# Kernel optimization log

Hardware: AMD Instinct MI355X
Metric: run time of the kernel (lower is better)

Reference implementation:

```python
import jax, jax.numpy as jnp
import numpy as np

NHEADS = 16
KVHEADS = 4
HEAD_DIM = 128  # emb_kq_per_head == emb_v_per_head
ROPE_THETA = 10000.0


def _rotary(x, cos, sin):
    # x: [B, S, H, D]; half-split rotation
    x1, x2 = jnp.split(x, 2, axis=-1)
    rot = jnp.concatenate([-x2, x1], axis=-1)
    return x * cos + rot * sin


def setup_inputs() -> dict:
    key = jax.random.key(0)
    k1, k2, k3 = jax.random.split(key, 3)
    B, S, E = 2, 2048, 2048
    qkv_out = NHEADS * HEAD_DIM + 2 * KVHEADS * HEAD_DIM  # 3072
    return {
        "x": jax.random.normal(k1, (B, S, E), dtype=jnp.float32),
        "w_qkv": jax.random.normal(k2, (E, qkv_out), dtype=jnp.float32) * 0.02,
        "w_dense": jax.random.normal(k3, (NHEADS * HEAD_DIM, E), dtype=jnp.float32) * 0.02,
    }


def reference(x, w_qkv, w_dense):
    B, S, E = x.shape
    D = HEAD_DIM
    # fused QKV projection (use_bias=False), then split per FusedQKV.splits
    qkv = x @ w_qkv  # [B, S, 3072]
    q, k, v = jnp.split(qkv, [NHEADS * D, NHEADS * D + KVHEADS * D], axis=-1)
    q = q.reshape(B, S, NHEADS, D)
    k = k.reshape(B, S, KVHEADS, D)
    v = v.reshape(B, S, KVHEADS, D)

    # rotary position encoding, positions = arange(S)
    pos = jnp.arange(S, dtype=jnp.float32)
    inv_freq = 1.0 / (ROPE_THETA ** (jnp.arange(0, D, 2, dtype=jnp.float32) / D))
    ang = pos[:, None] * inv_freq[None, :]                 # [S, D/2]
    ang = jnp.concatenate([ang, ang], axis=-1)             # [S, D]
    cos = jnp.cos(ang)[None, :, None, :]                   # [1, S, 1, D]
    sin = jnp.sin(ang)[None, :, None, :]
    q = _rotary(q, cos, sin)
    k = _rotary(k, cos, sin)

    # GQA: expand kv heads to query heads
    rep = NHEADS // KVHEADS
    k = jnp.repeat(k, rep, axis=2)  # [B, S, NHEADS, D]
    v = jnp.repeat(v, rep, axis=2)

    scale = 1.0 / jnp.sqrt(jnp.asarray(D, dtype=x.dtype))
    scores = jnp.einsum("bqhd,bkhd->bhqk", q, k) * scale   # [B, H, S, S]
    causal = jnp.tril(jnp.ones((S, S), dtype=bool))
    scores = jnp.where(causal[None, None], scores, jnp.finfo(scores.dtype).min)
    probs = jax.nn.softmax(scores, axis=-1)
    attn = jnp.einsum("bhqk,bkhd->bqhd", probs, v)         # [B, S, H, D]
    attn = attn.reshape(B, S, NHEADS * D)
    return attn @ w_dense                                  # [B, S, E]
```

## Files before the change

kernel.cpp:

```cpp
#include <hip/hip_runtime.h>
#include <type_traits>


typedef __attribute__((ext_vector_type(8))) short short8;
typedef __attribute__((ext_vector_type(4))) float floatx4;
typedef __attribute__((ext_vector_type(4))) unsigned short ushort4v;

constexpr int NH    = 16;
constexpr int NKV   = 4;
constexpr int HD    = 128;
constexpr int SEQ   = 2048;
constexpr int EMB   = 2048;
constexpr int NBATCH = 2;
constexpr int MROWS = NBATCH * SEQ;
constexpr int NQKV  = (NH + 2 * NKV) * HD;

__device__ __forceinline__ unsigned short f2b(float f) {
  union { float f; unsigned u; } v; v.f = f;
  unsigned u = v.u + 0x7FFFu + ((v.u >> 16) & 1u);
  return (unsigned short)(u >> 16);
}
__device__ __forceinline__ float b2f(unsigned short h) {
  union { unsigned u; float f; } v; v.u = (unsigned)h << 16;
  return v.f;
}

__device__ __forceinline__ void gload_lds16(const unsigned short* g,
                                            unsigned short* lds) {
  __builtin_amdgcn_global_load_lds(
      (const __attribute__((address_space(1))) unsigned int*)g,
      (__attribute__((address_space(3))) unsigned int*)lds, 16, 0, 0);
}

__global__ void cvt_f32_bf16(const float* __restrict__ in,
                             unsigned short* __restrict__ out, int n) {
  int i = (blockIdx.x * 256 + threadIdx.x) * 4;
  if (i + 3 < n) {
    floatx4 v = *(const floatx4*)(in + i);
    ushort4v o = { f2b(v[0]), f2b(v[1]), f2b(v[2]), f2b(v[3]) };
    *(ushort4v*)(out + i) = o;
  }
}

__global__ void transpose_cvt_f32(const float* __restrict__ in,
                                  unsigned short* __restrict__ out,
                                  int R, int C) {
  __shared__ float t[32][33];
  int c0 = blockIdx.x * 32, r0 = blockIdx.y * 32;
  int tx = threadIdx.x & 31, ty = threadIdx.x >> 5;
#pragma unroll
  for (int i = 0; i < 32; i += 8)
    t[ty + i][tx] = in[(long)(r0 + ty + i) * C + (c0 + tx)];
  __syncthreads();
#pragma unroll
  for (int i = 0; i < 32; i += 8)
    out[(long)(c0 + ty + i) * R + (r0 + tx)] = f2b(t[tx][ty + i]);
}

__global__ void transpose_bf16(const unsigned short* __restrict__ in,
                               unsigned short* __restrict__ out,
                               int R, int C) {
  __shared__ unsigned short t[32][34];
  long base = (long)blockIdx.z * R * C;
  in += base; out += base;
  int c0 = blockIdx.x * 32, r0 = blockIdx.y * 32;
  int tx = threadIdx.x & 31, ty = threadIdx.x >> 5;
#pragma unroll
  for (int i = 0; i < 32; i += 8)
    t[ty + i][tx] = in[(long)(r0 + ty + i) * C + (c0 + tx)];
  __syncthreads();
#pragma unroll
  for (int i = 0; i < 32; i += 8)
    out[(long)(c0 + ty + i) * R + (r0 + tx)] = t[tx][ty + i];
}

__global__ void rope_kernel(unsigned short* __restrict__ buf, float scale) {
  int idx = blockIdx.x * 256 + threadIdx.x;
  int i = idx & 63;
  int s = (idx >> 6) & (SEQ - 1);
  int bh = idx >> 17;
  unsigned short* p = buf + ((long)bh * SEQ + s) * HD;
  float e = -(float)i * (2.0f * 13.287712379549449f / 128.0f);
  float ang = (float)s * exp2f(e);
  float sn, c;
  sincosf(ang, &sn, &c);
  float x1 = b2f(p[i]), x2 = b2f(p[i + 64]);
  p[i]      = f2b((x1 * c - x2 * sn) * scale);
  p[i + 64] = f2b((x2 * c + x1 * sn) * scale);
}

constexpr int BM = 128, BN = 128, BK = 64;

template <int MODE>
__global__ __launch_bounds__(256, 2) void gemm_bt(
    const unsigned short* __restrict__ A,
    const unsigned short* __restrict__ BT,
    int Mdim, int Ndim, int Kdim,
    float* __restrict__ outF,
    unsigned short* __restrict__ Qb,
    unsigned short* __restrict__ Kb,
    unsigned short* __restrict__ Vb) {
  __shared__ __align__(16) unsigned short smem[BM * BK + BN * BK];
  unsigned short (*As)[BK] = (unsigned short (*)[BK])smem;
  unsigned short (*Bs)[BK] = (unsigned short (*)[BK])(smem + BM * BK);
  const int tid = threadIdx.x;
  const int bm = blockIdx.y * BM;
  const int bn = blockIdx.x * BN;
  const int wave = tid >> 6, lane = tid & 63;
  const int l = lane & 15, q = lane >> 4;
  const int wm = (wave >> 1) * 64, wn = (wave & 1) * 64;

  floatx4 acc[4][4] = {};

  const int srow = lane >> 3;
  const int scol = (lane & 7) * 8;
  const unsigned short* Arow = A + (long)bm * Kdim;
  const unsigned short* Brow = BT + (long)bn * Kdim;

  for (int k0 = 0; k0 < Kdim; k0 += BK) {
#pragma unroll
    for (int i = 0; i < 4; ++i) {
      const int r0 = wave * 32 + i * 8;
      gload_lds16(Arow + (long)(r0 + srow) * Kdim + k0 + scol, &As[r0][0]);
      gload_lds16(Brow + (long)(r0 + srow) * Kdim + k0 + scol, &Bs[r0][0]);
    }
    __syncthreads();
#pragma unroll
    for (int kk = 0; kk < 2; ++kk) {
      short8 af[4], bfr[4];
#pragma unroll
      for (int mi = 0; mi < 4; ++mi)
        af[mi] = *(const short8*)&As[wm + mi * 16 + l][kk * 32 + q * 8];
#pragma unroll
      for (int ni = 0; ni < 4; ++ni)
        bfr[ni] = *(const short8*)&Bs[wn + ni * 16 + l][kk * 32 + q * 8];
#pragma unroll
      for (int mi = 0; mi < 4; ++mi)
#pragma unroll
        for (int ni = 0; ni < 4; ++ni)
          acc[mi][ni] = __builtin_amdgcn_mfma_f32_16x16x32_bf16(
              af[mi], bfr[ni], acc[mi][ni], 0, 0, 0);
    }
    __syncthreads();
  }

  if constexpr (MODE == 1) {
#pragma unroll
    for (int mi = 0; mi < 4; ++mi) {
      const int rowbase = bm + wm + mi * 16 + q * 4;
#pragma unroll
      for (int ni = 0; ni < 4; ++ni) {
        const int col = bn + wn + ni * 16 + l;
#pragma unroll
        for (int r = 0; r < 4; ++r)
          outF[(long)(rowbase + r) * Ndim + col] = acc[mi][ni][r];
      }
    }
  } else {
    unsigned short (*Ct)[128] = (unsigned short (*)[128])smem;
#pragma unroll
    for (int mi = 0; mi < 4; ++mi)
#pragma unroll
      for (int ni = 0; ni < 4; ++ni)
#pragma unroll
        for (int r = 0; r < 4; ++r) {
          const int row = wm + mi * 16 + q * 4 + r;
          const int col = wn + ni * 16 + l;
          const int cs = ((((col >> 3) ^ row) & 7) | (col & 64 ? 8 : 0)) * 8 + (col & 7);
          Ct[row][cs] = f2b(acc[mi][ni][r]);
        }
    __syncthreads();
    const int row = tid >> 1, g = tid & 1;
    const int m = bm + row, bb = m >> 11, s = m & (SEQ - 1);
    unsigned short* dst;
    if (bn < NH * HD)
      dst = Qb + (((long)(bb * NH + (bn >> 7))) * SEQ + s) * HD;
    else if (bn < (NH + NKV) * HD)
      dst = Kb + (((long)(bb * NKV + ((bn - NH * HD) >> 7))) * SEQ + s) * HD;
    else
      dst = Vb + (((long)(bb * NKV + ((bn - (NH + NKV) * HD) >> 7))) * SEQ + s) * HD;
#pragma unroll
    for (int i = 0; i < 8; ++i) {
      const int blk = (g * 8) + (i ^ (row & 7));
      *(short8*)(dst + g * 64 + i * 8) = *(const short8*)&Ct[row][blk * 8];
    }
  }
}

__global__ __launch_bounds__(256, 2) void attn_kernel(
    const unsigned short* __restrict__ Q,
    const unsigned short* __restrict__ K,
    const unsigned short* __restrict__ VT,
    unsigned short* __restrict__ attn) {
  const int pair = blockIdx.x, h = blockIdx.y, b = blockIdx.z;
  const int kvh = h >> 2;
  const int tid = threadIdx.x;
  const int wave = tid >> 6, lane = tid & 63;
  const int l = lane & 15, q = lane >> 4;
  const int l7 = l & 7;
  const int wq = wave * 16;

  const unsigned short* Kh = K + ((long)(b * NKV + kvh)) * SEQ * HD;
  const unsigned short* VTh = VT + ((long)(b * NKV + kvh)) * HD * SEQ;

  __shared__ __align__(16) unsigned short Ks[2][64 * 128];
  __shared__ __align__(16) unsigned short VTs[2][144 * 64];
  __shared__ __align__(16) unsigned short Ps[64][72];

  int koff[4], voff[4];
  {
    const int k_rl = lane >> 4, k_bp = lane & 15;
    const int v_rl = lane >> 3, v_bp = lane & 7;
#pragma unroll
    for (int j = 0; j < 4; ++j) {
      const int rk = (wave * 4 + j) * 4 + k_rl;
      koff[j] = rk * HD + (k_bp ^ (rk & 15)) * 8;
      const int rv = (wave * 4 + j) * 8 + v_rl;
      voff[j] = rv * SEQ + (v_bp ^ (rv & 7)) * 8;
    }
  }

  {
    short8 onesv;
#pragma unroll
    for (int i = 0; i < 8; ++i) onesv[i] = (short)0x3F80;
    const int t8 = tid * 8;
    unsigned short* dstp = (t8 < 1024) ? &VTs[0][128 * 64 + t8]
                                       : &VTs[1][128 * 64 + (t8 - 1024)];
    *(short8*)dstp = onesv;
  }

  auto stage = [&](int c, int buf) {
    const unsigned short* kc = Kh + c * (64 * HD);
    const unsigned short* vc = VTh + c * 64;
#pragma unroll
    for (int j = 0; j < 4; ++j)
      gload_lds16(kc + koff[j], &Ks[buf][(wave * 4 + j) * 4 * 128]);
#pragma unroll
    for (int j = 0; j < 4; ++j)
      gload_lds16(vc + voff[j], &VTs[buf][(wave * 4 + j) * 8 * 64]);
  };

  auto chunk_body = [&](auto masked, int cur, int kv0, int qt,
                        short8* qf, floatx4* o, float* mrow) {
    constexpr bool MASKED = decltype(masked)::value;
    floatx4 sf[4] = {};
#pragma unroll
    for (int kk = 0; kk < 4; ++kk) {
      short8 kf[4];
#pragma unroll
      for (int ni = 0; ni < 4; ++ni) {
        const int row = ni * 16 + l;
        kf[ni] = *(const short8*)&Ks[cur][row * 128 + (((kk * 4 + q) ^ l) * 8)];
      }
#pragma unroll
      for (int ni = 0; ni < 4; ++ni)
        sf[ni] = __builtin_amdgcn_mfma_f32_16x16x32_bf16(
            qf[kk], kf[ni], sf[ni], 0, 0, 0);
    }
    float alpha[4], mloc[4];
#pragma unroll
    for (int r = 0; r < 4; ++r) {
      if constexpr (MASKED) {
        const int qrow = qt * 64 + wq + q * 4 + r;
#pragma unroll
        for (int ni = 0; ni < 4; ++ni)
          if (kv0 + ni * 16 + l > qrow) sf[ni][r] = -3e38f;
      }
      float smax = fmaxf(fmaxf(sf[0][r], sf[1][r]), fmaxf(sf[2][r], sf[3][r]));
#pragma unroll
      for (int d = 1; d < 16; d <<= 1) smax = fmaxf(smax, __shfl_xor(smax, d));
      const float mnew = fmaxf(mrow[r], smax);
      alpha[r] = exp2f(mrow[r] - mnew);
      mrow[r] = mnew;
      mloc[r] = mnew;
    }
    floatx4 av = { alpha[0], alpha[1], alpha[2], alpha[3] };
#pragma unroll
    for (int di = 0; di < 9; ++di) o[di] *= av;
#pragma unroll
    for (int r = 0; r < 4; ++r)
#pragma unroll
      for (int ni = 0; ni < 4; ++ni)
        Ps[wq + q * 4 + r][ni * 16 + l] = f2b(exp2f(sf[ni][r] - mloc[r]));
#pragma unroll
    for (int kvk = 0; kvk < 2; ++kvk) {
      short8 pf = *(const short8*)&Ps[wq + l][kvk * 32 + q * 8];
#pragma unroll
      for (int di = 0; di < 9; ++di) {
        const int row = di * 16 + l;
        short8 vf = *(const short8*)&VTs[cur][row * 64 + (((kvk * 4 + q) ^ l7) * 8)];
        o[di] = __builtin_amdgcn_mfma_f32_16x16x32_bf16(pf, vf, o[di], 0, 0, 0);
      }
    }
  };

#pragma unroll 1
  for (int half = 0; half < 2; ++half) {
    const int qt = half ? (31 - pair) : pair;
    const unsigned short* Qh = Q + (((long)(b * NH + h)) * SEQ + qt * 64) * HD;

    short8 qf[4];
#pragma unroll
    for (int kk = 0; kk < 4; ++kk)
      qf[kk] = *(const short8*)(Qh + (long)(wq + l) * HD + kk * 32 + q * 8);

    floatx4 o[9] = {};
    float mrow[4];
#pragma unroll
    for (int r = 0; r < 4; ++r) mrow[r] = -3e38f;

    const int nchunk = qt + 1;

    stage(0, 0);
    __syncthreads();

    int c = 0;
#pragma unroll 1
    for (; c < nchunk - 1; ++c) {
      stage(c + 1, (c & 1) ^ 1);
      chunk_body(std::false_type{}, c & 1, c * 64, qt, qf, o, mrow);
      __syncthreads();
    }
    chunk_body(std::true_type{}, c & 1, c * 64, qt, qf, o, mrow);
    __syncthreads();

#pragma unroll
    for (int r = 0; r < 4; ++r) {
      const float inv = 1.0f / o[8][r];
      const int s = qt * 64 + wq + q * 4 + r;
      unsigned short* dst = attn + ((long)(b * SEQ + s)) * (NH * HD) + h * HD;
#pragma unroll
      for (int di = 0; di < 8; ++di)
        dst[di * 16 + l] = f2b(o[di][r] * inv);
    }
  }
}

extern "C" void kernel_launch(void* const* d_in, const int* in_sizes, int n_in,
                              void* d_out, int out_size, void* d_ws, size_t ws_size,
                              hipStream_t stream) {
  const float* x       = (const float*)d_in[0];
  const float* w_qkv   = (const float*)d_in[1];
  const float* w_dense = (const float*)d_in[2];
  float* out = (float*)d_out;

  char* ws = (char*)d_ws;
  const size_t MB = 1024 * 1024;
  unsigned short* xb    = (unsigned short*)(ws);
  unsigned short* wqkvT = (unsigned short*)(ws + 16 * MB);
  unsigned short* wdT   = (unsigned short*)(ws + 28 * MB);
  unsigned short* Qb    = (unsigned short*)(ws + 36 * MB);
  unsigned short* Kb    = (unsigned short*)(ws + 52 * MB);
  unsigned short* Vb    = (unsigned short*)(ws + 56 * MB);
  unsigned short* VTb   = (unsigned short*)(ws + 60 * MB);
  unsigned short* attn  = xb;

  const float qscale = 0.08838834764831845f * 1.4426950408889634f;

  cvt_f32_bf16<<<(MROWS * EMB) / (256 * 4), 256, 0, stream>>>(x, xb, MROWS * EMB);
  transpose_cvt_f32<<<dim3(NQKV / 32, EMB / 32), 256, 0, stream>>>(w_qkv, wqkvT, EMB, NQKV);
  transpose_cvt_f32<<<dim3(EMB / 32, (NH * HD) / 32), 256, 0, stream>>>(w_dense, wdT, NH * HD, EMB);

  gemm_bt<0><<<dim3(NQKV / BN, MROWS / BM), 256, 0, stream>>>(
      xb, wqkvT, MROWS, NQKV, EMB, nullptr, Qb, Kb, Vb);

  rope_kernel<<<(NBATCH * NH * SEQ * 64) / 256, 256, 0, stream>>>(Qb, qscale);
  rope_kernel<<<(NBATCH * NKV * SEQ * 64) / 256, 256, 0, stream>>>(Kb, 1.0f);

  transpose_bf16<<<dim3(HD / 32, SEQ / 32, NBATCH * NKV), 256, 0, stream>>>(Vb, VTb, SEQ, HD);

  attn_kernel<<<dim3(16, NH, NBATCH), 256, 0, stream>>>(Qb, Kb, VTb, attn);

  gemm_bt<1><<<dim3(EMB / BN, MROWS / BM), 256, 0, stream>>>(
      attn, wdT, MROWS, EMB, NH * HD, out, nullptr, nullptr, nullptr);
}
```

Measured before the change: 329.3 us.

## Read V directly from global in attention, one q-tile per block, merge rope launches

The attention kernel stops staging the transposed V tile in shared memory and instead loads V fragments straight from global memory into registers for the PV MFMAs. The row-sum column becomes an MFMA against a register vector of ones. Each block now handles a single query tile, heaviest first, instead of a balanced pair, doubling the grid and raising launch bounds to 3 blocks per CU thanks to the smaller LDS footprint. The two rope launches are merged into one. The risk is uncoalesced, higher-latency global V reads repeated by every wave, which is also 4x redundant across GQA heads.

```diff
diff --git a/kernel.cpp b/kernel.cpp
--- a/kernel.cpp
+++ b/kernel.cpp
@@ -74,12 +74,16 @@
     out[(long)(c0 + ty + i) * R + (r0 + tx)] = t[tx][ty + i];
 }
 
-__global__ void rope_kernel(unsigned short* __restrict__ buf, float scale) {
+__global__ void rope_kernel(unsigned short* __restrict__ Qb,
+                            unsigned short* __restrict__ Kb, float qscale) {
   int idx = blockIdx.x * 256 + threadIdx.x;
   int i = idx & 63;
   int s = (idx >> 6) & (SEQ - 1);
   int bh = idx >> 17;
-  unsigned short* p = buf + ((long)bh * SEQ + s) * HD;
+  unsigned short* p;
+  float scale;
+  if (bh < NBATCH * NH) { p = Qb + ((long)bh * SEQ + s) * HD; scale = qscale; }
+  else { p = Kb + ((long)(bh - NBATCH * NH) * SEQ + s) * HD; scale = 1.0f; }
   float e = -(float)i * (2.0f * 13.287712379549449f / 128.0f);
   float ang = (float)s * exp2f(e);
   float sn, c;
@@ -187,61 +191,48 @@
   }
 }
 
-__global__ __launch_bounds__(256, 2) void attn_kernel(
+__global__ __launch_bounds__(256, 3) void attn_kernel(
     const unsigned short* __restrict__ Q,
     const unsigned short* __restrict__ K,
     const unsigned short* __restrict__ VT,
     unsigned short* __restrict__ attn) {
-  const int pair = blockIdx.x, h = blockIdx.y, b = blockIdx.z;
+  const int qt = 31 - blockIdx.x, h = blockIdx.y, b = blockIdx.z;
   const int kvh = h >> 2;
   const int tid = threadIdx.x;
   const int wave = tid >> 6, lane = tid & 63;
   const int l = lane & 15, q = lane >> 4;
-  const int l7 = l & 7;
   const int wq = wave * 16;
 
   const unsigned short* Kh = K + ((long)(b * NKV + kvh)) * SEQ * HD;
   const unsigned short* VTh = VT + ((long)(b * NKV + kvh)) * HD * SEQ;
 
   __shared__ __align__(16) unsigned short Ks[2][64 * 128];
-  __shared__ __align__(16) unsigned short VTs[2][144 * 64];
   __shared__ __align__(16) unsigned short Ps[64][72];
 
-  int koff[4], voff[4];
+  int koff[4];
   {
     const int k_rl = lane >> 4, k_bp = lane & 15;
-    const int v_rl = lane >> 3, v_bp = lane & 7;
 #pragma unroll
     for (int j = 0; j < 4; ++j) {
       const int rk = (wave * 4 + j) * 4 + k_rl;
       koff[j] = rk * HD + (k_bp ^ (rk & 15)) * 8;
-      const int rv = (wave * 4 + j) * 8 + v_rl;
-      voff[j] = rv * SEQ + (v_bp ^ (rv & 7)) * 8;
-    }
-  }
-
-  {
-    short8 onesv;
-#pragma unroll
-    for (int i = 0; i < 8; ++i) onesv[i] = (short)0x3F80;
-    const int t8 = tid * 8;
-    unsigned short* dstp = (t8 < 1024) ? &VTs[0][128 * 64 + t8]
-                                       : &VTs[1][128 * 64 + (t8 - 1024)];
-    *(short8*)dstp = onesv;
-  }
+    }
+  }
+
+  short8 onesf;
+#pragma unroll
+  for (int i = 0; i < 8; ++i) onesf[i] = (short)0x3F80;
 
   auto stage = [&](int c, int buf) {
     const unsigned short* kc = Kh + c * (64 * HD);
-    const unsigned short* vc = VTh + c * 64;
 #pragma unroll
     for (int j = 0; j < 4; ++j)
       gload_lds16(kc + koff[j], &Ks[buf][(wave * 4 + j) * 4 * 128]);
-#pragma unroll
-    for (int j = 0; j < 4; ++j)
-      gload_lds16(vc + voff[j], &VTs[buf][(wave * 4 + j) * 8 * 64]);
   };
 
-  auto chunk_body = [&](auto masked, int cur, int kv0, int qt,
+  const unsigned short* vbase = VTh + (long)l * SEQ + q * 8;
+
+  auto chunk_body = [&](auto masked, int cur, int kv0,
                         short8* qf, floatx4* o, float* mrow) {
     constexpr bool MASKED = decltype(masked)::value;
     floatx4 sf[4] = {};
@@ -283,57 +274,52 @@
 #pragma unroll
       for (int ni = 0; ni < 4; ++ni)
         Ps[wq + q * 4 + r][ni * 16 + l] = f2b(exp2f(sf[ni][r] - mloc[r]));
+    const unsigned short* vc = vbase + kv0;
 #pragma unroll
     for (int kvk = 0; kvk < 2; ++kvk) {
       short8 pf = *(const short8*)&Ps[wq + l][kvk * 32 + q * 8];
 #pragma unroll
-      for (int di = 0; di < 9; ++di) {
-        const int row = di * 16 + l;
-        short8 vf = *(const short8*)&VTs[cur][row * 64 + (((kvk * 4 + q) ^ l7) * 8)];
+      for (int di = 0; di < 8; ++di) {
+        short8 vf = *(const short8*)(vc + (long)di * (16 * SEQ) + kvk * 32);
         o[di] = __builtin_amdgcn_mfma_f32_16x16x32_bf16(pf, vf, o[di], 0, 0, 0);
       }
+      o[8] = __builtin_amdgcn_mfma_f32_16x16x32_bf16(pf, onesf, o[8], 0, 0, 0);
     }
   };
 
+  const unsigned short* Qh = Q + (((long)(b * NH + h)) * SEQ + qt * 64) * HD;
+  short8 qf[4];
+#pragma unroll
+  for (int kk = 0; kk < 4; ++kk)
+    qf[kk] = *(const short8*)(Qh + (long)(wq + l) * HD + kk * 32 + q * 8);
+
+  floatx4 o[9] = {};
+  float mrow[4];
+#pragma unroll
+  for (int r = 0; r < 4; ++r) mrow[r] = -3e38f;
+
+  const int nchunk = qt + 1;
+
+  stage(0, 0);
+  __syncthreads();
+
+  int c = 0;
 #pragma unroll 1
-  for (int half = 0; half < 2; ++half) {
-    const int qt = half ? (31 - pair) : pair;
-    const unsigned short* Qh = Q + (((long)(b * NH + h)) * SEQ + qt * 64) * HD;
-
-    short8 qf[4];
-#pragma unroll
-    for (int kk = 0; kk < 4; ++kk)
-      qf[kk] = *(const short8*)(Qh + (long)(wq + l) * HD + kk * 32 + q * 8);
-
-    floatx4 o[9] = {};
-    float mrow[4];
-#pragma unroll
-    for (int r = 0; r < 4; ++r) mrow[r] = -3e38f;
-
-    const int nchunk = qt + 1;
-
-    stage(0, 0);
+  for (; c < nchunk - 1; ++c) {
+    stage(c + 1, (c & 1) ^ 1);
+    chunk_body(std::false_type{}, c & 1, c * 64, qf, o, mrow);
     __syncthreads();
-
-    int c = 0;
-#pragma unroll 1
-    for (; c < nchunk - 1; ++c) {
-      stage(c + 1, (c & 1) ^ 1);
-      chunk_body(std::false_type{}, c & 1, c * 64, qt, qf, o, mrow);
-      __syncthreads();
-    }
-    chunk_body(std::true_type{}, c & 1, c * 64, qt, qf, o, mrow);
-    __syncthreads();
-
-#pragma unroll
-    for (int r = 0; r < 4; ++r) {
-      const float inv = 1.0f / o[8][r];
-      const int s = qt * 64 + wq + q * 4 + r;
-      unsigned short* dst = attn + ((long)(b * SEQ + s)) * (NH * HD) + h * HD;
-#pragma unroll
-      for (int di = 0; di < 8; ++di)
-        dst[di * 16 + l] = f2b(o[di][r] * inv);
-    }
+  }
+  chunk_body(std::true_type{}, c & 1, c * 64, qf, o, mrow);
+
+#pragma unroll
+  for (int r = 0; r < 4; ++r) {
+    const float inv = 1.0f / o[8][r];
+    const int s = qt * 64 + wq + q * 4 + r;
+    unsigned short* dst = attn + ((long)(b * SEQ + s)) * (NH * HD) + h * HD;
+#pragma unroll
+    for (int di = 0; di < 8; ++di)
+      dst[di * 16 + l] = f2b(o[di][r] * inv);
   }
 }
 
@@ -365,12 +351,11 @@
   gemm_bt<0><<<dim3(NQKV / BN, MROWS / BM), 256, 0, stream>>>(
       xb, wqkvT, MROWS, NQKV, EMB, nullptr, Qb, Kb, Vb);
 
-  rope_kernel<<<(NBATCH * NH * SEQ * 64) / 256, 256, 0, stream>>>(Qb, qscale);
-  rope_kernel<<<(NBATCH * NKV * SEQ * 64) / 256, 256, 0, stream>>>(Kb, 1.0f);
+  rope_kernel<<<(NBATCH * (NH + NKV) * SEQ * 64) / 256, 256, 0, stream>>>(Qb, Kb, qscale);
 
   transpose_bf16<<<dim3(HD / 32, SEQ / 32, NBATCH * NKV), 256, 0, stream>>>(Vb, VTb, SEQ, HD);
 
-  attn_kernel<<<dim3(16, NH, NBATCH), 256, 0, stream>>>(Qb, Kb, VTb, attn);
+  attn_kernel<<<dim3(32, NH, NBATCH), 256, 0, stream>>>(Qb, Kb, VTb, attn);
 
   gemm_bt<1><<<dim3(EMB / BN, MROWS / BM), 256, 0, stream>>>(
       attn, wdT, MROWS, EMB, NH * HD, out, nullptr, nullptr, nullptr);
```

After: 573.2 us. +74.1%, slower.
